# Kernel optimization log

Hardware: AMD Instinct MI355X
Metric: run time of the kernel (lower is better)

Reference implementation:

```python
import jax, jax.numpy as jnp
import numpy as np


def _gcn_conv(x, edge_index, edge_weight, W, b, n_nodes):
    # PyG GCNConv with normalize=True: add self-loops (weight 1), symmetric norm,
    # transform then aggregate: out[col] += norm * (x @ W)[row], plus bias.
    row = jnp.concatenate([edge_index[0], jnp.arange(n_nodes)])
    col = jnp.concatenate([edge_index[1], jnp.arange(n_nodes)])
    w = jnp.concatenate([edge_weight, jnp.ones((n_nodes,), x.dtype)])
    deg = jax.ops.segment_sum(w, col, num_segments=n_nodes)
    dinv = jnp.where(deg > 0, jax.lax.rsqrt(jnp.maximum(deg, 1e-12)), 0.0)
    norm = dinv[row] * w * dinv[col]            # [E+N]
    h = x @ W                                   # [N, out]
    msg = h[row] * norm[:, None]                # [E+N, out]
    out = jax.ops.segment_sum(msg, col, num_segments=n_nodes)
    return out + b


def setup_inputs() -> dict:
    key = jax.random.key(0)
    ks = jax.random.split(key, 6)
    N, E, F_IN, H, C = 50000, 800000, 512, 128, 40
    features = jax.random.normal(ks[0], (N, F_IN), jnp.float32)
    edge_index = jax.random.randint(ks[1], (2, E), 0, N, jnp.int64)
    edge_weight = jax.random.uniform(ks[2], (E,), jnp.float32)
    W1 = jax.random.normal(ks[3], (F_IN, H), jnp.float32) * 0.05
    b1 = jnp.zeros((H,), jnp.float32)
    W2 = jax.random.normal(ks[4], (H, C), jnp.float32) * 0.05
    b2 = jnp.zeros((C,), jnp.float32)
    return {"features": features, "edge_index": edge_index, "edge_weight": edge_weight,
            "W1": W1, "b1": b1, "W2": W2, "b2": b2}


def reference(features, edge_index, edge_weight, W1, b1, W2, b2):
    n_nodes = features.shape[0]
    x = _gcn_conv(features, edge_index, edge_weight, W1, b1, n_nodes)
    x = jax.nn.relu(x)
    # F.dropout(training=self.training): identity in eval mode
    x = _gcn_conv(x, edge_index, edge_weight, W2, b2, n_nodes)
    return jax.nn.log_softmax(x, axis=1)
```

## Files before the change

### kernel.cpp

```cpp
#include <hip/hip_runtime.h>
#include <math.h>

#define FIN  512
#define HDIM 128
#define CDIM 40
#define CPAD 48
#define CAP  64

typedef __attribute__((ext_vector_type(8))) short shortx8;
typedef __attribute__((ext_vector_type(4))) float f32x4;
typedef __attribute__((ext_vector_type(2))) float floatx2;

__device__ inline unsigned short f2bf(float x) {
    unsigned u = __builtin_bit_cast(unsigned, x);
    unsigned r = u + 0x7fffu + ((u >> 16) & 1u);
    return (unsigned short)(r >> 16);
}
__device__ inline float bfu(unsigned short v) { return __builtin_bit_cast(float, (unsigned)v << 16); }
__device__ inline float wdec(unsigned p) { return __builtin_bit_cast(float, (p & 0x7fffu) << 16); }
__device__ inline unsigned char f2fp8(float x) {
    return (unsigned char)(__builtin_amdgcn_cvt_pk_fp8_f32(x, x, 0, false) & 0xff);
}
__device__ inline floatx2 fp8x2_dec(unsigned short v) {
    return __builtin_amdgcn_cvt_pk_f32_fp8((int)(unsigned)v, false);
}

#define PREPB 280
__global__ void k_fill(const int* __restrict__ row, const int* __restrict__ col,
                       const float* __restrict__ w,
                       unsigned long long* __restrict__ cursor,
                       unsigned* __restrict__ bkt, int E, int eblocks,
                       const float* __restrict__ W1, const float* __restrict__ W2,
                       unsigned short* __restrict__ W1T, unsigned short* __restrict__ W2T) {
    if ((int)blockIdx.x >= eblocks) {
        const int i = ((int)blockIdx.x - eblocks) * 256 + (int)threadIdx.x;
        if (i < FIN * HDIM) {
            const int k = i >> 7, nn = i & 127;
            W1T[nn * FIN + k] = f2bf(W1[i]);
        } else {
            const int j = i - FIN * HDIM;
            const int nn = j >> 7, k = j & 127;
            W2T[j] = (nn < CDIM) ? f2bf(W2[k * CDIM + nn]) : (unsigned short)0;
        }
        return;
    }
    const int e = blockIdx.x * blockDim.x + threadIdx.x;
    if (e >= E) return;
    const int c = col[e];
    const float we = w[e];
    const unsigned long long wfix = (unsigned long long)(we * 4294967296.0f);
    const unsigned long long old = atomicAdd(&cursor[c], (1ULL << 40) | wfix);
    const int p = (int)(old >> 40);
    const unsigned wb = (__builtin_bit_cast(unsigned, we) + 0x8000u) >> 16;
    if (p < CAP) bkt[(size_t)c * CAP + p] = ((unsigned)row[e] << 15) | (wb & 0x7fffu);
}

__global__ void k_prep(const unsigned long long* __restrict__ cursor,
                       int* __restrict__ cnt, float* __restrict__ dinv, int n) {
    const int i = blockIdx.x * 256 + threadIdx.x;
    if (i < n) {
        const unsigned long long p = cursor[i];
        cnt[i] = min((int)(p >> 40), CAP);
        const float wsum = (float)(p & ((1ULL << 40) - 1)) * 2.3283064365386963e-10f;
        dinv[i] = rsqrtf(1.0f + wsum);
    }
}

#define G1_LDA 72
__global__ __launch_bounds__(256) void k_gemm1(const float* __restrict__ A,
                                               const unsigned short* __restrict__ W1T,
                                               const float* __restrict__ dinv,
                                               unsigned char* __restrict__ h1f8, int M) {
    __shared__ short As[64 * G1_LDA];
    __shared__ short Bs[128 * G1_LDA];
    const int tid  = threadIdx.x;
    const int wave = tid >> 6;
    const int lane = tid & 63;
    const int quad = lane >> 4;
    const int mr   = lane & 15;
    const int n0w  = wave * 32;
    const int m0b  = blockIdx.x * 64;

    const int srowA = tid >> 2, spartA = tid & 3;
    const int srowB = tid >> 1, spartB = tid & 1;

    f32x4 acc[4][2];
#pragma unroll
    for (int i = 0; i < 4; i++)
#pragma unroll
        for (int j = 0; j < 2; j++) acc[i][j] = (f32x4)0.f;

    const int growA = m0b + srowA;
    const bool okA = growA < M;
    const float* ap = A + (size_t)growA * FIN + spartA * 16;
    const unsigned short* bp = W1T + (size_t)srowB * FIN + spartB * 32;

    for (int k0 = 0; k0 < FIN; k0 += 64) {
#pragma unroll
        for (int i = 0; i < 2; i++) {
            float4 v0 = make_float4(0.f, 0.f, 0.f, 0.f), v1 = v0;
            if (okA) {
                v0 = *(const float4*)(ap + k0 + i * 8);
                v1 = *(const float4*)(ap + k0 + i * 8 + 4);
            }
            shortx8 pk;
            pk[0] = (short)f2bf(v0.x); pk[1] = (short)f2bf(v0.y);
            pk[2] = (short)f2bf(v0.z); pk[3] = (short)f2bf(v0.w);
            pk[4] = (short)f2bf(v1.x); pk[5] = (short)f2bf(v1.y);
            pk[6] = (short)f2bf(v1.z); pk[7] = (short)f2bf(v1.w);
            *(shortx8*)&As[srowA * G1_LDA + spartA * 16 + i * 8] = pk;
        }
#pragma unroll
        for (int i = 0; i < 4; i++)
            *(shortx8*)&Bs[srowB * G1_LDA + spartB * 32 + i * 8] =
                *(const shortx8*)(bp + k0 + i * 8);
        __syncthreads();

#pragma unroll
        for (int kk = 0; kk < 2; kk++) {
            shortx8 af[4], bfr[2];
#pragma unroll
            for (int mt = 0; mt < 4; mt++)
                af[mt] = *(shortx8*)&As[(mt * 16 + mr) * G1_LDA + kk * 32 + quad * 8];
#pragma unroll
            for (int nt = 0; nt < 2; nt++)
                bfr[nt] = *(shortx8*)&Bs[(n0w + nt * 16 + mr) * G1_LDA + kk * 32 + quad * 8];
#pragma unroll
            for (int mt = 0; mt < 4; mt++)
#pragma unroll
                for (int nt = 0; nt < 2; nt++)
                    acc[mt][nt] = __builtin_amdgcn_mfma_f32_16x16x32_bf16(
                        af[mt], bfr[nt], acc[mt][nt], 0, 0, 0);
        }
        __syncthreads();
    }
#pragma unroll
    for (int mt = 0; mt < 4; mt++)
#pragma unroll
        for (int r = 0; r < 4; r++) {
            const int om = m0b + mt * 16 + quad * 4 + r;
            if (om < M) {
                const float dv = dinv[om];
#pragma unroll
                for (int nt = 0; nt < 2; nt++)
                    h1f8[(size_t)om * HDIM + n0w + nt * 16 + mr] = f2fp8(dv * acc[mt][nt][r]);
            }
        }
}

#define G2_LDA 136
__global__ __launch_bounds__(256) void k_g1g2(
    const int* __restrict__ cnt_arr, const unsigned* __restrict__ bkt,
    const unsigned char* __restrict__ h1f8,
    const float* __restrict__ dinv, const float* __restrict__ b1,
    const unsigned short* __restrict__ W2T,
    unsigned short* __restrict__ h2a, unsigned short* __restrict__ h2b,
    int n_nodes) {
    __shared__ short Xs[64 * G2_LDA];
    const int tid  = threadIdx.x;
    const int wave = tid >> 6;
    const int lane = tid & 63;
    const int loff = lane * 2;
    const int m0b  = blockIdx.x * 64;
    const float bias0 = b1[loff], bias1 = b1[loff + 1];

    for (int i = 0; i < 16; i++) {
        const int node = m0b + wave * 16 + i;
        unsigned val = 0u;
        if (node < n_nodes) {
            const int cnt = cnt_arr[node];
            const unsigned* base = bkt + (size_t)node * CAP;
            float a0 = 0.f, a1 = 0.f, c0 = 0.f, c1 = 0.f;
            int s = 0;
            for (; s + 8 <= cnt; s += 8) {
                const uint4 qa = *(const uint4*)(base + s);
                const uint4 qb = *(const uint4*)(base + s + 4);
                const unsigned short v0 = *(const unsigned short*)(h1f8 + (size_t)(qa.x >> 15) * HDIM + loff);
                const unsigned short v1 = *(const unsigned short*)(h1f8 + (size_t)(qa.y >> 15) * HDIM + loff);
                const unsigned short v2 = *(const unsigned short*)(h1f8 + (size_t)(qa.z >> 15) * HDIM + loff);
                const unsigned short v3 = *(const unsigned short*)(h1f8 + (size_t)(qa.w >> 15) * HDIM + loff);
                const unsigned short v4 = *(const unsigned short*)(h1f8 + (size_t)(qb.x >> 15) * HDIM + loff);
                const unsigned short v5 = *(const unsigned short*)(h1f8 + (size_t)(qb.y >> 15) * HDIM + loff);
                const unsigned short v6 = *(const unsigned short*)(h1f8 + (size_t)(qb.z >> 15) * HDIM + loff);
                const unsigned short v7 = *(const unsigned short*)(h1f8 + (size_t)(qb.w >> 15) * HDIM + loff);
                const floatx2 f0 = fp8x2_dec(v0), f1 = fp8x2_dec(v1), f2 = fp8x2_dec(v2), f3 = fp8x2_dec(v3);
                const floatx2 f4 = fp8x2_dec(v4), f5 = fp8x2_dec(v5), f6 = fp8x2_dec(v6), f7 = fp8x2_dec(v7);
                a0 += wdec(qa.x) * f0.x + wdec(qa.y) * f1.x + wdec(qa.z) * f2.x + wdec(qa.w) * f3.x;
                a1 += wdec(qa.x) * f0.y + wdec(qa.y) * f1.y + wdec(qa.z) * f2.y + wdec(qa.w) * f3.y;
                c0 += wdec(qb.x) * f4.x + wdec(qb.y) * f5.x + wdec(qb.z) * f6.x + wdec(qb.w) * f7.x;
                c1 += wdec(qb.x) * f4.y + wdec(qb.y) * f5.y + wdec(qb.z) * f6.y + wdec(qb.w) * f7.y;
            }
            for (; s + 4 <= cnt; s += 4) {
                const uint4 qa = *(const uint4*)(base + s);
                const unsigned short v0 = *(const unsigned short*)(h1f8 + (size_t)(qa.x >> 15) * HDIM + loff);
                const unsigned short v1 = *(const unsigned short*)(h1f8 + (size_t)(qa.y >> 15) * HDIM + loff);
                const unsigned short v2 = *(const unsigned short*)(h1f8 + (size_t)(qa.z >> 15) * HDIM + loff);
                const unsigned short v3 = *(const unsigned short*)(h1f8 + (size_t)(qa.w >> 15) * HDIM + loff);
                const floatx2 f0 = fp8x2_dec(v0), f1 = fp8x2_dec(v1), f2 = fp8x2_dec(v2), f3 = fp8x2_dec(v3);
                a0 += wdec(qa.x) * f0.x + wdec(qa.y) * f1.x + wdec(qa.z) * f2.x + wdec(qa.w) * f3.x;
                a1 += wdec(qa.x) * f0.y + wdec(qa.y) * f1.y + wdec(qa.z) * f2.y + wdec(qa.w) * f3.y;
            }
            for (; s < cnt; s++) {
                const unsigned p = base[s];
                const unsigned short v = *(const unsigned short*)(h1f8 + (size_t)(p >> 15) * HDIM + loff);
                const floatx2 f = fp8x2_dec(v);
                a0 += wdec(p) * f.x;
                a1 += wdec(p) * f.y;
            }
            a0 += c0; a1 += c1;
            const float dl = dinv[node];
            const unsigned short vs = *(const unsigned short*)(h1f8 + (size_t)node * HDIM + loff);
            const floatx2 fs = fp8x2_dec(vs);
            a0 = fmaxf(dl * (a0 + fs.x) + bias0, 0.f);
            a1 = fmaxf(dl * (a1 + fs.y) + bias1, 0.f);
            val = (unsigned)f2bf(a0) | ((unsigned)f2bf(a1) << 16);
        }
        *(unsigned*)&Xs[(wave * 16 + i) * G2_LDA + loff] = val;
    }
    __syncthreads();

    const int quad = lane >> 4;
    const int mr   = lane & 15;
    f32x4 acc[3];
#pragma unroll
    for (int nt = 0; nt < 3; nt++) acc[nt] = (f32x4)0.f;
#pragma unroll
    for (int kk = 0; kk < 4; kk++) {
        const shortx8 af = *(const shortx8*)&Xs[(wave * 16 + mr) * G2_LDA + kk * 32 + quad * 8];
#pragma unroll
        for (int nt = 0; nt < 3; nt++) {
            const shortx8 bfr = *(const shortx8*)(W2T + (size_t)(nt * 16 + mr) * HDIM + kk * 32 + quad * 8);
            acc[nt] = __builtin_amdgcn_mfma_f32_16x16x32_bf16(af, bfr, acc[nt], 0, 0, 0);
        }
    }
#pragma unroll
    for (int r = 0; r < 4; r++) {
        const int om = m0b + wave * 16 + quad * 4 + r;
        if (om < n_nodes) {
            const float dv = dinv[om];
#pragma unroll
            for (int nt = 0; nt < 2; nt++)
                h2a[(size_t)om * 32 + nt * 16 + mr] = f2bf(dv * acc[nt][r]);
            if (mr < 8)
                h2b[(size_t)om * 8 + mr] = f2bf(dv * acc[2][r]);
        }
    }
}

__global__ __launch_bounds__(256) void k_gather2(
    const int* __restrict__ cnt_arr, const unsigned* __restrict__ bkt,
    const unsigned short* __restrict__ h2a, const unsigned short* __restrict__ h2b,
    const float* __restrict__ dinv, const float* __restrict__ b2,
    float* __restrict__ out, int n_nodes) {
    const int node = blockIdx.x * 4 + (threadIdx.x >> 6);
    const int lane = threadIdx.x & 63;
    if (node >= n_nodes) return;
    const bool act = lane < CDIM;
    const int cnt = cnt_arr[node];
    const unsigned* base = bkt + (size_t)node * CAP;
    const unsigned short* hb = (lane < 32) ? (h2a + lane) : (h2b + (lane & 31 & 7));
    const int hstride = (lane < 32) ? 32 : 8;
    float acc = 0.f, accb = 0.f;
    int s = 0;
    for (; s + 4 <= cnt; s += 4) {
        const uint4 q = *(const uint4*)(base + s);
        if (act) {
            acc  += wdec(q.x) * bfu(hb[(size_t)(q.x >> 15) * hstride])
                  + wdec(q.y) * bfu(hb[(size_t)(q.y >> 15) * hstride]);
            accb += wdec(q.z) * bfu(hb[(size_t)(q.z >> 15) * hstride])
                  + wdec(q.w) * bfu(hb[(size_t)(q.w >> 15) * hstride]);
        }
    }
    for (; s < cnt; s++) {
        const unsigned p = base[s];
        if (act) acc += wdec(p) * bfu(hb[(size_t)(p >> 15) * hstride]);
    }
    acc += accb;
    if (act) {
        const float dl = dinv[node];
        acc = dl * (acc + bfu(hb[(size_t)node * hstride])) + b2[lane];
    }
    float m = act ? acc : -INFINITY;
#pragma unroll
    for (int off = 32; off; off >>= 1) m = fmaxf(m, __shfl_xor(m, off));
    float se = act ? expf(acc - m) : 0.f;
#pragma unroll
    for (int off = 32; off; off >>= 1) se += __shfl_xor(se, off);
    if (act) out[(size_t)node * CDIM + lane] = acc - m - logf(se);
}

extern "C" void kernel_launch(void* const* d_in, const int* in_sizes, int n_in,
                              void* d_out, int out_size, void* d_ws, size_t ws_size,
                              hipStream_t stream) {
    const float* features = (const float*)d_in[0];
    const int*   eidx     = (const int*)d_in[1];
    const float* ew       = (const float*)d_in[2];
    const float* W1       = (const float*)d_in[3];
    const float* b1       = (const float*)d_in[4];
    const float* W2       = (const float*)d_in[5];
    const float* b2       = (const float*)d_in[6];
    float* out = (float*)d_out;

    const int Nn = in_sizes[0] / FIN;
    const int E  = in_sizes[2];
    const int* row = eidx;
    const int* col = eidx + E;

    char* ws = (char*)d_ws;
    size_t off = 0;
    auto alloc = [&](size_t bytes) { void* p = ws + off; off += (bytes + 255) & ~(size_t)255; return p; };
    unsigned long long* cursor = (unsigned long long*)alloc((size_t)Nn * 8);
    int*      cnt          = (int*)     alloc((size_t)Nn * 4);
    float*    dinv         = (float*)   alloc((size_t)Nn * 4);
    unsigned* bkt          = (unsigned*)alloc((size_t)Nn * CAP * 4);
    unsigned short* W1T    = (unsigned short*)alloc((size_t)FIN * HDIM * 2);
    unsigned short* W2T    = (unsigned short*)alloc((size_t)CPAD * HDIM * 2);
    unsigned char*  h1f8   = (unsigned char*) alloc((size_t)Nn * HDIM);
    unsigned short* h2a    = (unsigned short*)alloc((size_t)Nn * 32 * 2);
    unsigned short* h2b    = (unsigned short*)alloc((size_t)Nn * 8 * 2);

    const int eblocks = (E + 255) / 256;

    hipMemsetAsync(cursor, 0, (size_t)Nn * 8, stream);
    k_fill<<<eblocks + PREPB, 256, 0, stream>>>(row, col, ew, cursor, bkt, E, eblocks,
                                                W1, W2, W1T, W2T);
    k_prep<<<(Nn + 255) / 256, 256, 0, stream>>>(cursor, cnt, dinv, Nn);
    k_gemm1<<<(Nn + 63) / 64, 256, 0, stream>>>(features, W1T, dinv, h1f8, Nn);
    k_g1g2<<<(Nn + 63) / 64, 256, 0, stream>>>(cnt, bkt, h1f8, dinv, b1, W2T,
                                               h2a, h2b, Nn);
    k_gather2<<<(Nn + 3) / 4, 256, 0, stream>>>(cnt, bkt, h2a, h2b, dinv, b2, out, Nn);
}
```

Before: 333.7 us.

## Assign one node per wave in fused gather-GEMM kernel with 1024-thread blocks

Restructures k_g1g2 so each of 16 waves in a 1024-thread block gathers one node, instead of each of 4 waves serially gathering 16 nodes. This exposes far more independent gather latency in parallel and removes the serial per-wave node loop. The small second GEMM is then split across three waves, one per 16-column output tile, while the other 13 waves idle. The trade-offs are the extra block-level barrier cost on large blocks and possible occupancy limits from 1024-thread launch bounds.

Result: faster. 313.9 us (-5.9%).

```diff
diff --git a/kernel.cpp b/kernel.cpp
--- a/kernel.cpp
+++ b/kernel.cpp
@@ -149,100 +149,92 @@
 }
 
 #define G2_LDA 136
-__global__ __launch_bounds__(256) void k_g1g2(
+__global__ __launch_bounds__(1024) void k_g1g2(
     const int* __restrict__ cnt_arr, const unsigned* __restrict__ bkt,
     const unsigned char* __restrict__ h1f8,
     const float* __restrict__ dinv, const float* __restrict__ b1,
     const unsigned short* __restrict__ W2T,
     unsigned short* __restrict__ h2a, unsigned short* __restrict__ h2b,
     int n_nodes) {
-    __shared__ short Xs[64 * G2_LDA];
+    __shared__ short Xs[16 * G2_LDA];
     const int tid  = threadIdx.x;
     const int wave = tid >> 6;
     const int lane = tid & 63;
     const int loff = lane * 2;
-    const int m0b  = blockIdx.x * 64;
-    const float bias0 = b1[loff], bias1 = b1[loff + 1];
-
-    for (int i = 0; i < 16; i++) {
-        const int node = m0b + wave * 16 + i;
-        unsigned val = 0u;
-        if (node < n_nodes) {
-            const int cnt = cnt_arr[node];
-            const unsigned* base = bkt + (size_t)node * CAP;
-            float a0 = 0.f, a1 = 0.f, c0 = 0.f, c1 = 0.f;
-            int s = 0;
-            for (; s + 8 <= cnt; s += 8) {
-                const uint4 qa = *(const uint4*)(base + s);
-                const uint4 qb = *(const uint4*)(base + s + 4);
-                const unsigned short v0 = *(const unsigned short*)(h1f8 + (size_t)(qa.x >> 15) * HDIM + loff);
-                const unsigned short v1 = *(const unsigned short*)(h1f8 + (size_t)(qa.y >> 15) * HDIM + loff);
-                const unsigned short v2 = *(const unsigned short*)(h1f8 + (size_t)(qa.z >> 15) * HDIM + loff);
-                const unsigned short v3 = *(const unsigned short*)(h1f8 + (size_t)(qa.w >> 15) * HDIM + loff);
-                const unsigned short v4 = *(const unsigned short*)(h1f8 + (size_t)(qb.x >> 15) * HDIM + loff);
-                const unsigned short v5 = *(const unsigned short*)(h1f8 + (size_t)(qb.y >> 15) * HDIM + loff);
-                const unsigned short v6 = *(const unsigned short*)(h1f8 + (size_t)(qb.z >> 15) * HDIM + loff);
-                const unsigned short v7 = *(const unsigned short*)(h1f8 + (size_t)(qb.w >> 15) * HDIM + loff);
-                const floatx2 f0 = fp8x2_dec(v0), f1 = fp8x2_dec(v1), f2 = fp8x2_dec(v2), f3 = fp8x2_dec(v3);
-                const floatx2 f4 = fp8x2_dec(v4), f5 = fp8x2_dec(v5), f6 = fp8x2_dec(v6), f7 = fp8x2_dec(v7);
-                a0 += wdec(qa.x) * f0.x + wdec(qa.y) * f1.x + wdec(qa.z) * f2.x + wdec(qa.w) * f3.x;
-                a1 += wdec(qa.x) * f0.y + wdec(qa.y) * f1.y + wdec(qa.z) * f2.y + wdec(qa.w) * f3.y;
-                c0 += wdec(qb.x) * f4.x + wdec(qb.y) * f5.x + wdec(qb.z) * f6.x + wdec(qb.w) * f7.x;
-                c1 += wdec(qb.x) * f4.y + wdec(qb.y) * f5.y + wdec(qb.z) * f6.y + wdec(qb.w) * f7.y;
+    const int m0b  = blockIdx.x * 16;
+    const int node = m0b + wave;
+
+    unsigned val = 0u;
+    if (node < n_nodes) {
+        const int cnt = cnt_arr[node];
+        const unsigned* base = bkt + (size_t)node * CAP;
+        float a0 = 0.f, a1 = 0.f, c0 = 0.f, c1 = 0.f;
+        int s = 0;
+        for (; s + 8 <= cnt; s += 8) {
+            const uint4 qa = *(const uint4*)(base + s);
+            const uint4 qb = *(const uint4*)(base + s + 4);
+            const unsigned short v0 = *(const unsigned short*)(h1f8 + (size_t)(qa.x >> 15) * HDIM + loff);
+            const unsigned short v1 = *(const unsigned short*)(h1f8 + (size_t)(qa.y >> 15) * HDIM + loff);
+            const unsigned short v2 = *(const unsigned short*)(h1f8 + (size_t)(qa.z >> 15) * HDIM + loff);
+            const unsigned short v3 = *(const unsigned short*)(h1f8 + (size_t)(qa.w >> 15) * HDIM + loff);
+            const unsigned short v4 = *(const unsigned short*)(h1f8 + (size_t)(qb.x >> 15) * HDIM + loff);
+            const unsigned short v5 = *(const unsigned short*)(h1f8 + (size_t)(qb.y >> 15) * HDIM + loff);
+            const unsigned short v6 = *(const unsigned short*)(h1f8 + (size_t)(qb.z >> 15) * HDIM + loff);
+            const unsigned short v7 = *(const unsigned short*)(h1f8 + (size_t)(qb.w >> 15) * HDIM + loff);
+            const floatx2 f0 = fp8x2_dec(v0), f1 = fp8x2_dec(v1), f2 = fp8x2_dec(v2), f3 = fp8x2_dec(v3);
+            const floatx2 f4 = fp8x2_dec(v4), f5 = fp8x2_dec(v5), f6 = fp8x2_dec(v6), f7 = fp8x2_dec(v7);
+            a0 += wdec(qa.x) * f0.x + wdec(qa.y) * f1.x + wdec(qa.z) * f2.x + wdec(qa.w) * f3.x;
+            a1 += wdec(qa.x) * f0.y + wdec(qa.y) * f1.y + wdec(qa.z) * f2.y + wdec(qa.w) * f3.y;
+            c0 += wdec(qb.x) * f4.x + wdec(qb.y) * f5.x + wdec(qb.z) * f6.x + wdec(qb.w) * f7.x;
+            c1 += wdec(qb.x) * f4.y + wdec(qb.y) * f5.y + wdec(qb.z) * f6.y + wdec(qb.w) * f7.y;
+        }
+        for (; s + 4 <= cnt; s += 4) {
+            const uint4 qa = *(const uint4*)(base + s);
+            const unsigned short v0 = *(const unsigned short*)(h1f8 + (size_t)(qa.x >> 15) * HDIM + loff);
+            const unsigned short v1 = *(const unsigned short*)(h1f8 + (size_t)(qa.y >> 15) * HDIM + loff);
+            const unsigned short v2 = *(const unsigned short*)(h1f8 + (size_t)(qa.z >> 15) * HDIM + loff);
+            const unsigned short v3 = *(const unsigned short*)(h1f8 + (size_t)(qa.w >> 15) * HDIM + loff);
+            const floatx2 f0 = fp8x2_dec(v0), f1 = fp8x2_dec(v1), f2 = fp8x2_dec(v2), f3 = fp8x2_dec(v3);
+            a0 += wdec(qa.x) * f0.x + wdec(qa.y) * f1.x + wdec(qa.z) * f2.x + wdec(qa.w) * f3.x;
+            a1 += wdec(qa.x) * f0.y + wdec(qa.y) * f1.y + wdec(qa.z) * f2.y + wdec(qa.w) * f3.y;
+        }
+        for (; s < cnt; s++) {
+            const unsigned p = base[s];
+            const unsigned short v = *(const unsigned short*)(h1f8 + (size_t)(p >> 15) * HDIM + loff);
+            const floatx2 f = fp8x2_dec(v);
+            a0 += wdec(p) * f.x;
+            a1 += wdec(p) * f.y;
+        }
+        a0 += c0; a1 += c1;
+        const float dl = dinv[node];
+        const unsigned short vs = *(const unsigned short*)(h1f8 + (size_t)node * HDIM + loff);
+        const floatx2 fs = fp8x2_dec(vs);
+        a0 = fmaxf(dl * (a0 + fs.x) + b1[loff], 0.f);
+        a1 = fmaxf(dl * (a1 + fs.y) + b1[loff + 1], 0.f);
+        val = (unsigned)f2bf(a0) | ((unsigned)f2bf(a1) << 16);
+    }
+    *(unsigned*)&Xs[wave * G2_LDA + loff] = val;
+    __syncthreads();
+
+    if (wave < 3) {
+        const int quad = lane >> 4;
+        const int mr   = lane & 15;
+        const int nt   = wave;
+        f32x4 acc = (f32x4)0.f;
+#pragma unroll
+        for (int kk = 0; kk < 4; kk++) {
+            const shortx8 af  = *(const shortx8*)&Xs[mr * G2_LDA + kk * 32 + quad * 8];
+            const shortx8 bfr = *(const shortx8*)(W2T + (size_t)(nt * 16 + mr) * HDIM + kk * 32 + quad * 8);
+            acc = __builtin_amdgcn_mfma_f32_16x16x32_bf16(af, bfr, acc, 0, 0, 0);
+        }
+#pragma unroll
+        for (int r = 0; r < 4; r++) {
+            const int om = m0b + quad * 4 + r;
+            if (om < n_nodes) {
+                const float dv = dinv[om];
+                if (nt < 2)       h2a[(size_t)om * 32 + nt * 16 + mr] = f2bf(dv * acc[r]);
+                else if (mr < 8)  h2b[(size_t)om * 8 + mr] = f2bf(dv * acc[r]);
             }
-            for (; s + 4 <= cnt; s += 4) {
-                const uint4 qa = *(const uint4*)(base + s);
-                const unsigned short v0 = *(const unsigned short*)(h1f8 + (size_t)(qa.x >> 15) * HDIM + loff);
-                const unsigned short v1 = *(const unsigned short*)(h1f8 + (size_t)(qa.y >> 15) * HDIM + loff);
-                const unsigned short v2 = *(const unsigned short*)(h1f8 + (size_t)(qa.z >> 15) * HDIM + loff);
-                const unsigned short v3 = *(const unsigned short*)(h1f8 + (size_t)(qa.w >> 15) * HDIM + loff);
-                const floatx2 f0 = fp8x2_dec(v0), f1 = fp8x2_dec(v1), f2 = fp8x2_dec(v2), f3 = fp8x2_dec(v3);
-                a0 += wdec(qa.x) * f0.x + wdec(qa.y) * f1.x + wdec(qa.z) * f2.x + wdec(qa.w) * f3.x;
-                a1 += wdec(qa.x) * f0.y + wdec(qa.y) * f1.y + wdec(qa.z) * f2.y + wdec(qa.w) * f3.y;
-            }
-            for (; s < cnt; s++) {
-                const unsigned p = base[s];
-                const unsigned short v = *(const unsigned short*)(h1f8 + (size_t)(p >> 15) * HDIM + loff);
-                const floatx2 f = fp8x2_dec(v);
-                a0 += wdec(p) * f.x;
-                a1 += wdec(p) * f.y;
-            }
-            a0 += c0; a1 += c1;
-            const float dl = dinv[node];
-            const unsigned short vs = *(const unsigned short*)(h1f8 + (size_t)node * HDIM + loff);
-            const floatx2 fs = fp8x2_dec(vs);
-            a0 = fmaxf(dl * (a0 + fs.x) + bias0, 0.f);
-            a1 = fmaxf(dl * (a1 + fs.y) + bias1, 0.f);
-            val = (unsigned)f2bf(a0) | ((unsigned)f2bf(a1) << 16);
-        }
-        *(unsigned*)&Xs[(wave * 16 + i) * G2_LDA + loff] = val;
-    }
-    __syncthreads();
-
-    const int quad = lane >> 4;
-    const int mr   = lane & 15;
-    f32x4 acc[3];
-#pragma unroll
-    for (int nt = 0; nt < 3; nt++) acc[nt] = (f32x4)0.f;
-#pragma unroll
-    for (int kk = 0; kk < 4; kk++) {
-        const shortx8 af = *(const shortx8*)&Xs[(wave * 16 + mr) * G2_LDA + kk * 32 + quad * 8];
-#pragma unroll
-        for (int nt = 0; nt < 3; nt++) {
-            const shortx8 bfr = *(const shortx8*)(W2T + (size_t)(nt * 16 + mr) * HDIM + kk * 32 + quad * 8);
-            acc[nt] = __builtin_amdgcn_mfma_f32_16x16x32_bf16(af, bfr, acc[nt], 0, 0, 0);
-        }
-    }
-#pragma unroll
-    for (int r = 0; r < 4; r++) {
-        const int om = m0b + wave * 16 + quad * 4 + r;
-        if (om < n_nodes) {
-            const float dv = dinv[om];
-#pragma unroll
-            for (int nt = 0; nt < 2; nt++)
-                h2a[(size_t)om * 32 + nt * 16 + mr] = f2bf(dv * acc[nt][r]);
-            if (mr < 8)
-                h2b[(size_t)om * 8 + mr] = f2bf(dv * acc[2][r]);
         }
     }
 }
@@ -258,7 +250,7 @@
     const bool act = lane < CDIM;
     const int cnt = cnt_arr[node];
     const unsigned* base = bkt + (size_t)node * CAP;
-    const unsigned short* hb = (lane < 32) ? (h2a + lane) : (h2b + (lane & 31 & 7));
+    const unsigned short* hb = (lane < 32) ? (h2a + lane) : (h2b + (lane & 7));
     const int hstride = (lane < 32) ? 32 : 8;
     float acc = 0.f, accb = 0.f;
     int s = 0;
@@ -326,7 +318,7 @@
                                                 W1, W2, W1T, W2T);
     k_prep<<<(Nn + 255) / 256, 256, 0, stream>>>(cursor, cnt, dinv, Nn);
     k_gemm1<<<(Nn + 63) / 64, 256, 0, stream>>>(features, W1T, dinv, h1f8, Nn);
-    k_g1g2<<<(Nn + 63) / 64, 256, 0, stream>>>(cnt, bkt, h1f8, dinv, b1, W2T,
-                                               h2a, h2b, Nn);
+    k_g1g2<<<(Nn + 15) / 16, 1024, 0, stream>>>(cnt, bkt, h1f8, dinv, b1, W2T,
+                                                h2a, h2b, Nn);
     k_gather2<<<(Nn + 3) / 4, 256, 0, stream>>>(cnt, bkt, h2a, h2b, dinv, b2, out, Nn);
 }
```
